# Kernel optimization log

Hardware: AMD Instinct MI355X
Metric: run time of the kernel (lower is better)

The kernel has to match this reference:

```python
import jax, jax.numpy as jnp
import numpy as np

B = 64          # num_graphs per batch
ADJ = 1000      # adj_shape (nodes per graph)
N = B * ADJ     # total nodes
E = 1 << 20     # edges
M = 32000       # selected (batch, node) pairs
D_IN = 128
D_OUT = 128


def setup_inputs() -> dict:
    key = jax.random.key(0)
    ks = jax.random.split(key, 12)
    inp = {
        "x0": jax.random.normal(ks[0], (N, D_IN), jnp.float32),
        "x1": jax.random.normal(ks[1], (N, D_IN), jnp.float32),
        "edge_index": jax.random.randint(ks[2], (2, E), 0, N, jnp.int64),
        "b_idx0": jax.random.randint(ks[3], (M,), 0, B, jnp.int64),
        "n_idx0": jax.random.randint(ks[4], (M,), 0, ADJ, jnp.int64),
        "b_idx1": jax.random.randint(ks[5], (M,), 0, B, jnp.int64),
        "n_idx1": jax.random.randint(ks[6], (M,), 0, ADJ, jnp.int64),
        "W1": jax.random.normal(ks[7], (D_IN, D_IN), jnp.float32) / np.sqrt(D_IN),
        "b1": jnp.zeros((D_IN,), jnp.float32),
        "W2": jax.random.normal(ks[8], (D_IN, D_IN), jnp.float32) / np.sqrt(D_IN),
        "b2": jnp.zeros((D_IN,), jnp.float32),
        "Wl": jax.random.normal(ks[9], (D_IN, D_OUT), jnp.float32) / np.sqrt(D_IN),
        "bl": jnp.zeros((D_OUT,), jnp.float32),
        "Wfi": jax.random.normal(ks[10], (D_IN, D_OUT), jnp.float32) / np.sqrt(D_IN),
        "bfi": jnp.zeros((D_OUT,), jnp.float32),
    }
    return inp


def _gnn_layer(h, edge_index, W, b):
    # GCN-style message passing: gather source features, scatter-sum to dst,
    # then linear project.  h: [N, d]
    msgs = h[edge_index[0]]                                    # [E, d] gather
    agg = jax.ops.segment_sum(msgs, edge_index[1], num_segments=N)  # [N, d]
    return agg @ W + b


def reference(x0, x1, edge_index, b_idx0, n_idx0, b_idx1, n_idx1,
              W1, b1, W2, b2, Wl, bl, Wfi, bfi):
    # branch i == 0: raw features -> 2D gather -> fc_in
    d0 = x0.reshape(B, ADJ, -1)[b_idx0, n_idx0]                # [M, D_IN]
    d0 = d0 @ Wfi + bfi                                        # [M, D_OUT]

    # branch i == 1 (observ=True): gnn1 -> gnn2 -> 2D gather -> linear
    # (dropout omitted for deterministic reference; p=0.2 at train time)
    h = _gnn_layer(x1, edge_index, W1, b1)
    h = _gnn_layer(h, edge_index, W2, b2)
    d1 = h.reshape(B, ADJ, -1)[b_idx1, n_idx1]                 # [M, D_IN]
    d1 = d1 @ Wl + bl                                          # [M, D_OUT]

    return jnp.stack([d0, d1])                                 # [2, M, D_OUT]
```

## Files before the change

### kernel.cpp

```cpp
#include <hip/hip_runtime.h>
#include <hip/hip_bf16.h>


#define B_    64
#define ADJ_  1000
#define N_    64000
#define E_    (1 << 20)
#define M_    32000
#define DV    128
#define CAP   64
#define RANGES 8
#define RSPAN  (N_ / RANGES)
#define CHUNKS 512
#define EPB    (E_ / CHUNKS)

typedef __attribute__((ext_vector_type(8))) short short8v;
typedef __attribute__((ext_vector_type(4))) float float4v;

__device__ __forceinline__ float u2f(unsigned int u) {
  union { unsigned int i; float f; } x; x.i = u; return x.f;
}
__device__ __forceinline__ unsigned short f2bf(float f) {
  union { float f; unsigned int i; } x; x.f = f;
  unsigned int r = x.i + 0x7fffu + ((x.i >> 16) & 1u);
  return (unsigned short)(r >> 16);
}
__device__ __forceinline__ unsigned int pack_bf2(float a, float b) {
  __hip_bfloat162 h = __float22bfloat162_rn(float2{a, b});
  union { __hip_bfloat162 h; unsigned int u; } c; c.h = h;
  return c.u;
}

__device__ __forceinline__ void fill_part(const int* __restrict__ ei,
                                          int* __restrict__ counts,
                                          unsigned short* __restrict__ bucket,
                                          int c, int r) {
  const int* srcA = ei;
  const int* dstA = ei + E_;
  int lo = r * RSPAN;
  int t4 = c * EPB + (int)threadIdx.x * 4;
  int4 d0 = *(const int4*)(dstA + t4);
  int4 s0 = *(const int4*)(srcA + t4);
  int4 d1 = *(const int4*)(dstA + t4 + 1024);
  int4 s1 = *(const int4*)(srcA + t4 + 1024);
#define PROC(D, S) do {                                                \
    if ((unsigned)((D) - lo) < (unsigned)RSPAN) {                      \
      int pos = atomicAdd(&counts[(D)], 1);                            \
      if (pos < CAP) bucket[(D) * CAP + pos] = (unsigned short)(S);    \
    } } while (0)
  PROC(d0.x, s0.x); PROC(d0.y, s0.y); PROC(d0.z, s0.z); PROC(d0.w, s0.w);
  PROC(d1.x, s1.x); PROC(d1.y, s1.y); PROC(d1.z, s1.z); PROC(d1.w, s1.w);
#undef PROC
}

template<bool GATHER, bool ABF16, bool OUTBF16, bool HASBIAS>
__device__ __forceinline__ void gemm_tile(const void* __restrict__ in,
                                          const float* __restrict__ W,
                                          const float* __restrict__ bias,
                                          void* __restrict__ out_, int tile,
                                          const int* __restrict__ bidx,
                                          const int* __restrict__ nidx,
                                          unsigned short* __restrict__ Bs) {
  int tid = threadIdx.x;
#pragma unroll 8
  for (int i = 0; i < 64; i++) {
    int g = i * 256 + tid;
    int k = g >> 7, n = g & 127;
    int addr = ((((n >> 4) * 4 + (k >> 5)) * 64 + ((k >> 3) & 3) * 16 + (n & 15)) << 3)
             + (k & 7);
    Bs[addr] = f2bf(W[g]);
  }
  __syncthreads();

  int lane = tid & 63;
  int wv   = tid >> 6;
  int m    = lane & 15;
  int q    = lane >> 4;
  int rbase = tile * 64 + wv * 16;
  int r     = rbase + m;

  size_t ir;
  if (GATHER) ir = (size_t)bidx[r] * ADJ_ + nidx[r];
  else        ir = (size_t)r;

  short8v af[4];
  if (ABF16) {
    const unsigned short* arow = (const unsigned short*)in + ir * DV;
#pragma unroll
    for (int kc = 0; kc < 4; kc++)
      af[kc] = *(const short8v*)(arow + kc * 32 + q * 8);
  } else {
    const float* arow = (const float*)in + ir * DV;
#pragma unroll
    for (int kc = 0; kc < 4; kc++) {
      const float4* p = (const float4*)(arow + kc * 32 + q * 8);
      float4 f0 = p[0], f1 = p[1];
      union { short8v s; unsigned int u[4]; } t;
      t.u[0] = pack_bf2(f0.x, f0.y);
      t.u[1] = pack_bf2(f0.z, f0.w);
      t.u[2] = pack_bf2(f1.x, f1.y);
      t.u[3] = pack_bf2(f1.z, f1.w);
      af[kc] = t.s;
    }
  }

  float4v acc[8];
#pragma unroll
  for (int nb = 0; nb < 8; nb++) acc[nb] = (float4v){0.f, 0.f, 0.f, 0.f};
#pragma unroll
  for (int nb = 0; nb < 8; nb++)
#pragma unroll
    for (int kc = 0; kc < 4; kc++) {
      short8v bf = *(const short8v*)(Bs + (((nb * 4 + kc) * 64 + lane) << 3));
      acc[nb] = __builtin_amdgcn_mfma_f32_16x16x32_bf16(af[kc], bf, acc[nb], 0, 0, 0);
    }

#pragma unroll
  for (int nb = 0; nb < 8; nb++) {
    float bvn = HASBIAS ? bias[nb * 16 + m] : 0.f;
    int col = nb * 16 + m;
#pragma unroll
    for (int i = 0; i < 4; i++) {
      int row = rbase + q * 4 + i;
      float v = acc[nb][i] + bvn;
      if (OUTBF16) ((unsigned short*)out_)[(size_t)row * DV + col] = f2bf(v);
      else         ((float*)out_)[(size_t)row * DV + col] = v;
    }
  }
}

__global__ __launch_bounds__(256)
void k1_fused(const int* __restrict__ ei, int* __restrict__ counts,
              unsigned short* __restrict__ bucket,
              const float* __restrict__ x1, const float* __restrict__ W1,
              unsigned int* __restrict__ t_bf,
              const float* __restrict__ x0, const float* __restrict__ Wfi,
              const float* __restrict__ bfi, float* __restrict__ out0,
              const int* __restrict__ b0, const int* __restrict__ n0i) {
  __shared__ unsigned short Bs[16384];
  int g = blockIdx.x >> 4, rem = blockIdx.x & 15;
  if (rem < 8) { fill_part(ei, counts, bucket, g, rem); return; }
  int o = g * 8 + rem - 8;
  if (o < 1000)
    gemm_tile<false, false, true, false>(x1, W1, nullptr, t_bf, o, nullptr, nullptr, Bs);
  else if (o < 1500)
    gemm_tile<true, false, false, true>(x0, Wfi, bfi, out0, o - 1000, b0, n0i, Bs);
}

template<bool GATHER, bool ABF16, bool OUTBF16, bool HASBIAS>
__global__ __launch_bounds__(256)
void gemm_k(const void* __restrict__ in, const float* __restrict__ W,
            const float* __restrict__ bias, void* __restrict__ out_,
            const int* __restrict__ bidx, const int* __restrict__ nidx) {
  __shared__ unsigned short Bs[16384];
  gemm_tile<GATHER, ABF16, OUTBF16, HASBIAS>(in, W, bias, out_, blockIdx.x, bidx, nidx, Bs);
}

template<bool OUTBF16, bool SEL>
__global__ __launch_bounds__(256)
void aggregate_k(const unsigned int* __restrict__ x,
                 const int* __restrict__ counts,
                 const unsigned short* __restrict__ bucket,
                 const float* __restrict__ bias, void* __restrict__ out_,
                 const int* __restrict__ bidx, const int* __restrict__ nidx) {
  int w    = (blockIdx.x * 256 + threadIdx.x) >> 6;
  int lane = threadIdx.x & 63;
  int node = SEL ? (bidx[w] * ADJ_ + nidx[w]) : w;
  int cnt = counts[node]; cnt = min(cnt, CAP);
  int mysrc = (int)bucket[node * CAP + lane];
  float2 bv = ((const float2*)bias)[lane];
  float2 acc; acc.x = bv.x; acc.y = bv.y;

  int d = 0;
  for (; d + 4 <= cnt; d += 4) {
    int s0 = __shfl(mysrc, d, 64);
    int s1 = __shfl(mysrc, d + 1, 64);
    int s2 = __shfl(mysrc, d + 2, 64);
    int s3 = __shfl(mysrc, d + 3, 64);
    unsigned int u0 = x[(size_t)s0 * 64 + lane];
    unsigned int u1 = x[(size_t)s1 * 64 + lane];
    unsigned int u2 = x[(size_t)s2 * 64 + lane];
    unsigned int u3 = x[(size_t)s3 * 64 + lane];
    acc.x += (u2f(u0 << 16) + u2f(u1 << 16)) + (u2f(u2 << 16) + u2f(u3 << 16));
    acc.y += (u2f(u0 & 0xffff0000u) + u2f(u1 & 0xffff0000u))
           + (u2f(u2 & 0xffff0000u) + u2f(u3 & 0xffff0000u));
  }
  for (; d < cnt; d++) {
    int s = __shfl(mysrc, d, 64);
    unsigned int u = x[(size_t)s * 64 + lane];
    acc.x += u2f(u << 16);
    acc.y += u2f(u & 0xffff0000u);
  }
  if (OUTBF16) ((unsigned int*)out_)[(size_t)w * 64 + lane] = pack_bf2(acc.x, acc.y);
  else         ((float2*)out_)[(size_t)w * 64 + lane] = acc;
}

extern "C" void kernel_launch(void* const* d_in, const int* in_sizes, int n_in,
                              void* d_out, int out_size, void* d_ws, size_t ws_size,
                              hipStream_t stream) {
  const float* x0  = (const float*)d_in[0];
  const float* x1  = (const float*)d_in[1];
  const int*   ei  = (const int*)  d_in[2];
  const int*   b0  = (const int*)  d_in[3];
  const int*   n0i = (const int*)  d_in[4];
  const int*   b1  = (const int*)  d_in[5];
  const int*   n1i = (const int*)  d_in[6];
  const float* W1  = (const float*)d_in[7];
  const float* bb1 = (const float*)d_in[8];
  const float* W2  = (const float*)d_in[9];
  const float* bb2 = (const float*)d_in[10];
  const float* Wl  = (const float*)d_in[11];
  const float* bl  = (const float*)d_in[12];
  const float* Wfi = (const float*)d_in[13];
  const float* bfi = (const float*)d_in[14];
  float* out = (float*)d_out;

  unsigned int*   t_bf   = (unsigned int*)d_ws;
  unsigned int*   h_bf   = t_bf + (size_t)N_ * 64;
  unsigned int*   sel_bf = h_bf + (size_t)N_ * 64;
  int*            counts = (int*)(sel_bf + (size_t)M_ * 64);
  unsigned short* bucket = (unsigned short*)(counts + N_);

  hipMemsetAsync(counts, 0, N_ * sizeof(int), stream);

  k1_fused<<<512 * 16, 256, 0, stream>>>(ei, counts, bucket, x1, W1, t_bf,
                                         x0, Wfi, bfi, out, b0, n0i);

  aggregate_k<true, false><<<N_ / 4, 256, 0, stream>>>(t_bf, counts, bucket, bb1,
                                                       h_bf, nullptr, nullptr);
  gemm_k<false, true, true, false><<<N_ / 64, 256, 0, stream>>>(h_bf, W2, nullptr,
                                                                t_bf, nullptr, nullptr);
  aggregate_k<true, true><<<M_ / 4, 256, 0, stream>>>(t_bf, counts, bucket, bb2,
                                                      sel_bf, b1, n1i);
  gemm_k<false, true, false, true><<<M_ / 64, 256, 0, stream>>>(sel_bf, Wl, bl,
                                                                out + (size_t)M_ * DV,
                                                                nullptr, nullptr);
}
```

Measured before the change: 269.5 us.

## Fuse aggregation with following GEMM and pre-convert weights once in a prep kernel

Each neighbour aggregation is now fused with the linear projection after it: a block aggregates 64 rows into LDS as bf16 and then runs the MFMA GEMM directly, which removes the intermediate h/sel buffers and two kernel launches. A new prep kernel converts all four weight matrices to the swizzled bf16 layout once and zeroes the counts, replacing the memset and the per-block LDS weight conversion; GEMMs read B fragments from global memory instead. Edge-index loads become nontemporal. The fused kernel has fewer blocks with 16 serial rows per wave, which may reduce latency hiding in the gather phase.

```diff
diff --git a/kernel.cpp b/kernel.cpp
--- a/kernel.cpp
+++ b/kernel.cpp
@@ -16,6 +16,7 @@
 
 typedef __attribute__((ext_vector_type(8))) short short8v;
 typedef __attribute__((ext_vector_type(4))) float float4v;
+typedef __attribute__((ext_vector_type(4))) int   int4v;
 
 __device__ __forceinline__ float u2f(unsigned int u) {
   union { unsigned int i; float f; } x; x.i = u; return x.f;
@@ -29,6 +30,24 @@
   __hip_bfloat162 h = __float22bfloat162_rn(float2{a, b});
   union { __hip_bfloat162 h; unsigned int u; } c; c.h = h;
   return c.u;
+}
+
+__global__ __launch_bounds__(256)
+void prep(const float* __restrict__ W1, const float* __restrict__ W2,
+          const float* __restrict__ Wl, const float* __restrict__ Wfi,
+          unsigned short* __restrict__ wf, int* __restrict__ counts) {
+  int t = blockIdx.x * 256 + threadIdx.x;
+  if (t < 4 * 16384) {
+    int mtx = t >> 14, g = t & 16383;
+    const float* W = mtx == 0 ? W1 : mtx == 1 ? W2 : mtx == 2 ? Wl : Wfi;
+    int k = g >> 7, n = g & 127;
+    int addr = ((((n >> 4) * 4 + (k >> 5)) * 64 + ((k >> 3) & 3) * 16 + (n & 15)) << 3)
+             + (k & 7);
+    wf[mtx * 16384 + addr] = f2bf(W[g]);
+  } else {
+    int c = t - 65536;
+    if (c < N_) counts[c] = 0;
+  }
 }
 
 __device__ __forceinline__ void fill_part(const int* __restrict__ ei,
@@ -39,79 +58,55 @@
   const int* dstA = ei + E_;
   int lo = r * RSPAN;
   int t4 = c * EPB + (int)threadIdx.x * 4;
-  int4 d0 = *(const int4*)(dstA + t4);
-  int4 s0 = *(const int4*)(srcA + t4);
-  int4 d1 = *(const int4*)(dstA + t4 + 1024);
-  int4 s1 = *(const int4*)(srcA + t4 + 1024);
+  int4v d0 = __builtin_nontemporal_load((const int4v*)(dstA + t4));
+  int4v s0 = __builtin_nontemporal_load((const int4v*)(srcA + t4));
+  int4v d1 = __builtin_nontemporal_load((const int4v*)(dstA + t4 + 1024));
+  int4v s1 = __builtin_nontemporal_load((const int4v*)(srcA + t4 + 1024));
 #define PROC(D, S) do {                                                \
     if ((unsigned)((D) - lo) < (unsigned)RSPAN) {                      \
       int pos = atomicAdd(&counts[(D)], 1);                            \
-      if (pos < CAP) bucket[(D) * CAP + pos] = (unsigned short)(S);    \
+      if (pos < CAP) bucket[(size_t)(D) * CAP + pos] = (unsigned short)(S); \
     } } while (0)
   PROC(d0.x, s0.x); PROC(d0.y, s0.y); PROC(d0.z, s0.z); PROC(d0.w, s0.w);
   PROC(d1.x, s1.x); PROC(d1.y, s1.y); PROC(d1.z, s1.z); PROC(d1.w, s1.w);
 #undef PROC
 }
 
-template<bool GATHER, bool ABF16, bool OUTBF16, bool HASBIAS>
-__device__ __forceinline__ void gemm_tile(const void* __restrict__ in,
-                                          const float* __restrict__ W,
-                                          const float* __restrict__ bias,
-                                          void* __restrict__ out_, int tile,
-                                          const int* __restrict__ bidx,
-                                          const int* __restrict__ nidx,
-                                          unsigned short* __restrict__ Bs) {
-  int tid = threadIdx.x;
-#pragma unroll 8
-  for (int i = 0; i < 64; i++) {
-    int g = i * 256 + tid;
-    int k = g >> 7, n = g & 127;
-    int addr = ((((n >> 4) * 4 + (k >> 5)) * 64 + ((k >> 3) & 3) * 16 + (n & 15)) << 3)
-             + (k & 7);
-    Bs[addr] = f2bf(W[g]);
-  }
-  __syncthreads();
-
-  int lane = tid & 63;
-  int wv   = tid >> 6;
-  int m    = lane & 15;
-  int q    = lane >> 4;
+template<bool GATHER, bool OUTBF16, bool HASBIAS>
+__device__ __forceinline__ void gemm_g(const float* __restrict__ in,
+                                       const unsigned short* __restrict__ wf,
+                                       const float* __restrict__ bias,
+                                       void* __restrict__ out_, int tile,
+                                       const int* __restrict__ bidx,
+                                       const int* __restrict__ nidx) {
+  int lane = threadIdx.x & 63, wv = threadIdx.x >> 6;
+  int m = lane & 15, q = lane >> 4;
   int rbase = tile * 64 + wv * 16;
-  int r     = rbase + m;
-
-  size_t ir;
-  if (GATHER) ir = (size_t)bidx[r] * ADJ_ + nidx[r];
-  else        ir = (size_t)r;
+  int r = rbase + m;
+  size_t ir = GATHER ? (size_t)bidx[r] * ADJ_ + nidx[r] : (size_t)r;
+  const float* arow = in + ir * DV;
 
   short8v af[4];
-  if (ABF16) {
-    const unsigned short* arow = (const unsigned short*)in + ir * DV;
-#pragma unroll
-    for (int kc = 0; kc < 4; kc++)
-      af[kc] = *(const short8v*)(arow + kc * 32 + q * 8);
-  } else {
-    const float* arow = (const float*)in + ir * DV;
+#pragma unroll
+  for (int kc = 0; kc < 4; kc++) {
+    const float4* p = (const float4*)(arow + kc * 32 + q * 8);
+    float4 f0 = p[0], f1 = p[1];
+    union { short8v s; unsigned int u[4]; } t;
+    t.u[0] = pack_bf2(f0.x, f0.y);
+    t.u[1] = pack_bf2(f0.z, f0.w);
+    t.u[2] = pack_bf2(f1.x, f1.y);
+    t.u[3] = pack_bf2(f1.z, f1.w);
+    af[kc] = t.s;
+  }
+
+  float4v acc[8];
+#pragma unroll
+  for (int nb = 0; nb < 8; nb++) acc[nb] = (float4v){0.f, 0.f, 0.f, 0.f};
+#pragma unroll
+  for (int nb = 0; nb < 8; nb++)
 #pragma unroll
     for (int kc = 0; kc < 4; kc++) {
-      const float4* p = (const float4*)(arow + kc * 32 + q * 8);
-      float4 f0 = p[0], f1 = p[1];
-      union { short8v s; unsigned int u[4]; } t;
-      t.u[0] = pack_bf2(f0.x, f0.y);
-      t.u[1] = pack_bf2(f0.z, f0.w);
-      t.u[2] = pack_bf2(f1.x, f1.y);
-      t.u[3] = pack_bf2(f1.z, f1.w);
-      af[kc] = t.s;
-    }
-  }
-
-  float4v acc[8];
-#pragma unroll
-  for (int nb = 0; nb < 8; nb++) acc[nb] = (float4v){0.f, 0.f, 0.f, 0.f};
-#pragma unroll
-  for (int nb = 0; nb < 8; nb++)
-#pragma unroll
-    for (int kc = 0; kc < 4; kc++) {
-      short8v bf = *(const short8v*)(Bs + (((nb * 4 + kc) * 64 + lane) << 3));
+      short8v bf = *(const short8v*)(wf + (((nb * 4 + kc) * 64 + lane) << 3));
       acc[nb] = __builtin_amdgcn_mfma_f32_16x16x32_bf16(af[kc], bf, acc[nb], 0, 0, 0);
     }
 
@@ -130,69 +125,97 @@
 }
 
 __global__ __launch_bounds__(256)
-void k1_fused(const int* __restrict__ ei, int* __restrict__ counts,
-              unsigned short* __restrict__ bucket,
-              const float* __restrict__ x1, const float* __restrict__ W1,
-              unsigned int* __restrict__ t_bf,
-              const float* __restrict__ x0, const float* __restrict__ Wfi,
-              const float* __restrict__ bfi, float* __restrict__ out0,
-              const int* __restrict__ b0, const int* __restrict__ n0i) {
-  __shared__ unsigned short Bs[16384];
+void k1(const int* __restrict__ ei, int* __restrict__ counts,
+        unsigned short* __restrict__ bucket,
+        const float* __restrict__ x1, const unsigned short* __restrict__ wf1,
+        unsigned int* __restrict__ t1,
+        const float* __restrict__ x0, const unsigned short* __restrict__ wff,
+        const float* __restrict__ bfi, float* __restrict__ out0,
+        const int* __restrict__ b0, const int* __restrict__ n0i) {
   int g = blockIdx.x >> 4, rem = blockIdx.x & 15;
   if (rem < 8) { fill_part(ei, counts, bucket, g, rem); return; }
   int o = g * 8 + rem - 8;
   if (o < 1000)
-    gemm_tile<false, false, true, false>(x1, W1, nullptr, t_bf, o, nullptr, nullptr, Bs);
+    gemm_g<false, true, false>(x1, wf1, nullptr, t1, o, nullptr, nullptr);
   else if (o < 1500)
-    gemm_tile<true, false, false, true>(x0, Wfi, bfi, out0, o - 1000, b0, n0i, Bs);
-}
-
-template<bool GATHER, bool ABF16, bool OUTBF16, bool HASBIAS>
+    gemm_g<true, false, true>(x0, wff, bfi, out0, o - 1000, b0, n0i);
+}
+
+template<bool SEL, bool OUTBF16, bool BIAS2>
 __global__ __launch_bounds__(256)
-void gemm_k(const void* __restrict__ in, const float* __restrict__ W,
-            const float* __restrict__ bias, void* __restrict__ out_,
-            const int* __restrict__ bidx, const int* __restrict__ nidx) {
-  __shared__ unsigned short Bs[16384];
-  gemm_tile<GATHER, ABF16, OUTBF16, HASBIAS>(in, W, bias, out_, blockIdx.x, bidx, nidx, Bs);
-}
-
-template<bool OUTBF16, bool SEL>
-__global__ __launch_bounds__(256)
-void aggregate_k(const unsigned int* __restrict__ x,
-                 const int* __restrict__ counts,
-                 const unsigned short* __restrict__ bucket,
-                 const float* __restrict__ bias, void* __restrict__ out_,
-                 const int* __restrict__ bidx, const int* __restrict__ nidx) {
-  int w    = (blockIdx.x * 256 + threadIdx.x) >> 6;
-  int lane = threadIdx.x & 63;
-  int node = SEL ? (bidx[w] * ADJ_ + nidx[w]) : w;
-  int cnt = counts[node]; cnt = min(cnt, CAP);
-  int mysrc = (int)bucket[node * CAP + lane];
-  float2 bv = ((const float2*)bias)[lane];
-  float2 acc; acc.x = bv.x; acc.y = bv.y;
-
-  int d = 0;
-  for (; d + 4 <= cnt; d += 4) {
-    int s0 = __shfl(mysrc, d, 64);
-    int s1 = __shfl(mysrc, d + 1, 64);
-    int s2 = __shfl(mysrc, d + 2, 64);
-    int s3 = __shfl(mysrc, d + 3, 64);
-    unsigned int u0 = x[(size_t)s0 * 64 + lane];
-    unsigned int u1 = x[(size_t)s1 * 64 + lane];
-    unsigned int u2 = x[(size_t)s2 * 64 + lane];
-    unsigned int u3 = x[(size_t)s3 * 64 + lane];
-    acc.x += (u2f(u0 << 16) + u2f(u1 << 16)) + (u2f(u2 << 16) + u2f(u3 << 16));
-    acc.y += (u2f(u0 & 0xffff0000u) + u2f(u1 & 0xffff0000u))
-           + (u2f(u2 & 0xffff0000u) + u2f(u3 & 0xffff0000u));
-  }
-  for (; d < cnt; d++) {
-    int s = __shfl(mysrc, d, 64);
-    unsigned int u = x[(size_t)s * 64 + lane];
-    acc.x += u2f(u << 16);
-    acc.y += u2f(u & 0xffff0000u);
-  }
-  if (OUTBF16) ((unsigned int*)out_)[(size_t)w * 64 + lane] = pack_bf2(acc.x, acc.y);
-  else         ((float2*)out_)[(size_t)w * 64 + lane] = acc;
+void agg_gemm(const unsigned int* __restrict__ x,
+              const int* __restrict__ counts,
+              const unsigned short* __restrict__ bucket,
+              const float* __restrict__ bias1,
+              const unsigned short* __restrict__ wf,
+              const float* __restrict__ bias2, void* __restrict__ out_,
+              const int* __restrict__ bidx, const int* __restrict__ nidx) {
+  __shared__ unsigned int As[64 * 68];
+  int tid = threadIdx.x, lane = tid & 63, wv = tid >> 6;
+  int tile = blockIdx.x;
+  float2 bv = ((const float2*)bias1)[lane];
+
+  for (int i = 0; i < 16; i++) {
+    int rl = wv * 16 + i;
+    int grow = tile * 64 + rl;
+    int node = SEL ? (bidx[grow] * ADJ_ + nidx[grow]) : grow;
+    int cnt = counts[node]; cnt = min(cnt, CAP);
+    int mysrc = (int)bucket[(size_t)node * CAP + lane];
+    float accx = bv.x, accy = bv.y;
+    int d = 0;
+    for (; d + 4 <= cnt; d += 4) {
+      int s0 = __shfl(mysrc, d, 64);
+      int s1 = __shfl(mysrc, d + 1, 64);
+      int s2 = __shfl(mysrc, d + 2, 64);
+      int s3 = __shfl(mysrc, d + 3, 64);
+      unsigned int u0 = x[(size_t)s0 * 64 + lane];
+      unsigned int u1 = x[(size_t)s1 * 64 + lane];
+      unsigned int u2 = x[(size_t)s2 * 64 + lane];
+      unsigned int u3 = x[(size_t)s3 * 64 + lane];
+      accx += (u2f(u0 << 16) + u2f(u1 << 16)) + (u2f(u2 << 16) + u2f(u3 << 16));
+      accy += (u2f(u0 & 0xffff0000u) + u2f(u1 & 0xffff0000u))
+            + (u2f(u2 & 0xffff0000u) + u2f(u3 & 0xffff0000u));
+    }
+    for (; d < cnt; d++) {
+      int s = __shfl(mysrc, d, 64);
+      unsigned int u = x[(size_t)s * 64 + lane];
+      accx += u2f(u << 16);
+      accy += u2f(u & 0xffff0000u);
+    }
+    As[rl * 68 + lane] = pack_bf2(accx, accy);
+  }
+  __syncthreads();
+
+  int m = lane & 15, q = lane >> 4;
+  const unsigned short* As16 = (const unsigned short*)As;
+  short8v af[4];
+#pragma unroll
+  for (int kc = 0; kc < 4; kc++)
+    af[kc] = *(const short8v*)(As16 + (wv * 16 + m) * 136 + kc * 32 + q * 8);
+
+  float4v acc[8];
+#pragma unroll
+  for (int nb = 0; nb < 8; nb++) acc[nb] = (float4v){0.f, 0.f, 0.f, 0.f};
+#pragma unroll
+  for (int nb = 0; nb < 8; nb++)
+#pragma unroll
+    for (int kc = 0; kc < 4; kc++) {
+      short8v bf = *(const short8v*)(wf + (((nb * 4 + kc) * 64 + lane) << 3));
+      acc[nb] = __builtin_amdgcn_mfma_f32_16x16x32_bf16(af[kc], bf, acc[nb], 0, 0, 0);
+    }
+
+#pragma unroll
+  for (int nb = 0; nb < 8; nb++) {
+    float bvn = BIAS2 ? bias2[nb * 16 + m] : 0.f;
+    int col = nb * 16 + m;
+#pragma unroll
+    for (int i = 0; i < 4; i++) {
+      int row = tile * 64 + wv * 16 + q * 4 + i;
+      float v = acc[nb][i] + bvn;
+      if (OUTBF16) ((unsigned short*)out_)[(size_t)row * DV + col] = f2bf(v);
+      else         ((float*)out_)[(size_t)row * DV + col] = v;
+    }
+  }
 }
 
 extern "C" void kernel_launch(void* const* d_in, const int* in_sizes, int n_in,
@@ -215,24 +238,21 @@
   const float* bfi = (const float*)d_in[14];
   float* out = (float*)d_out;
 
-  unsigned int*   t_bf   = (unsigned int*)d_ws;
-  unsigned int*   h_bf   = t_bf + (size_t)N_ * 64;
-  unsigned int*   sel_bf = h_bf + (size_t)N_ * 64;
-  int*            counts = (int*)(sel_bf + (size_t)M_ * 64);
+  unsigned int*   t1     = (unsigned int*)d_ws;
+  unsigned int*   t2     = t1 + (size_t)N_ * 64;
+  int*            counts = (int*)(t2 + (size_t)N_ * 64);
   unsigned short* bucket = (unsigned short*)(counts + N_);
-
-  hipMemsetAsync(counts, 0, N_ * sizeof(int), stream);
-
-  k1_fused<<<512 * 16, 256, 0, stream>>>(ei, counts, bucket, x1, W1, t_bf,
-                                         x0, Wfi, bfi, out, b0, n0i);
-
-  aggregate_k<true, false><<<N_ / 4, 256, 0, stream>>>(t_bf, counts, bucket, bb1,
-                                                       h_bf, nullptr, nullptr);
-  gemm_k<false, true, true, false><<<N_ / 64, 256, 0, stream>>>(h_bf, W2, nullptr,
-                                                                t_bf, nullptr, nullptr);
-  aggregate_k<true, true><<<M_ / 4, 256, 0, stream>>>(t_bf, counts, bucket, bb2,
-                                                      sel_bf, b1, n1i);
-  gemm_k<false, true, false, true><<<M_ / 64, 256, 0, stream>>>(sel_bf, Wl, bl,
-                                                                out + (size_t)M_ * DV,
-                                                                nullptr, nullptr);
-}
+  unsigned short* wf     = bucket + (size_t)N_ * CAP;
+  unsigned short* wf1 = wf, *wf2 = wf + 16384, *wfl = wf + 32768, *wff = wf + 49152;
+
+  prep<<<(4 * 16384 + N_ + 255) / 256, 256, 0, stream>>>(W1, W2, Wl, Wfi, wf, counts);
+
+  k1<<<CHUNKS * 16, 256, 0, stream>>>(ei, counts, bucket, x1, wf1, t1,
+                                      x0, wff, bfi, out, b0, n0i);
+
+  agg_gemm<false, true, false><<<N_ / 64, 256, 0, stream>>>(
+      t1, counts, bucket, bb1, wf2, nullptr, t2, nullptr, nullptr);
+
+  agg_gemm<true, false, true><<<M_ / 64, 256, 0, stream>>>(
+      t2, counts, bucket, bb2, wfl, bl, out + (size_t)M_ * DV, b1, n1i);
+}
```

New measurement: 305.8 us. 1.13x slower.
